# Kernel tuning notes

Measured on AMD Instinct MI355X. Metric: run time of the kernel, lower is better.

## Reference

```python
import jax, jax.numpy as jnp
import numpy as np

N = 100_000   # nodes
D = 128       # in_channels
H = 128       # hidden_channels
O = 128       # out_channels
M = 3_200_000 # adjacency nnz (avg degree 32)
E = 200_000   # query edges
P = 500_000   # common-neighbor pairs (padded, all valid here)
COS_EPS = 1e-8
DEG_EPS = 1e-6


def setup_inputs() -> dict:
    key = jax.random.key(0)
    ks = jax.random.split(key, 12)
    x = jax.random.normal(ks[0], (N, D), jnp.float32)
    adj_row = jnp.sort(jax.random.randint(ks[1], (M,), 0, N, jnp.int32))
    adj_col = jax.random.randint(ks[2], (M,), 0, N, jnp.int32)
    edges = jax.random.randint(ks[3], (2, E), 0, N, jnp.int32)
    cn_edge_idx = jnp.sort(jax.random.randint(ks[4], (P,), 0, E, jnp.int32))
    cn_node = jax.random.randint(ks[5], (P,), 0, N, jnp.int32)
    cn_valid = jnp.ones((P,), jnp.bool_)
    # MLP params (Kaiming-ish scale)
    W1 = jax.random.normal(ks[6], (D, H), jnp.float32) / np.sqrt(D)
    b1 = jnp.zeros((H,), jnp.float32)
    W2 = jax.random.normal(ks[7], (H, H), jnp.float32) / np.sqrt(H)
    b2 = jnp.zeros((H,), jnp.float32)
    W3 = jax.random.normal(ks[8], (H, O), jnp.float32) / np.sqrt(H)
    b3 = jnp.zeros((O,), jnp.float32)
    return dict(x=x, adj_row=adj_row, adj_col=adj_col, edges=edges,
                cn_edge_idx=cn_edge_idx, cn_node=cn_node, cn_valid=cn_valid,
                W1=W1, b1=b1, W2=W2, b2=b2, W3=W3, b3=b3)


def _cosine(a, b):
    # torch.nn.CosineSimilarity: dot / max(||a||*||b||, eps)
    dot = jnp.sum(a * b, axis=-1)
    na = jnp.sqrt(jnp.sum(a * a, axis=-1))
    nb = jnp.sqrt(jnp.sum(b * b, axis=-1))
    return dot / jnp.maximum(na * nb, COS_EPS)


def reference(x, adj_row, adj_col, edges, cn_edge_idx, cn_node, cn_valid,
              W1, b1, W2, b2, W3, b3):
    # degrees = adj.sum(-1) + 1e-6 (binary adjacency values)
    ones = jnp.ones(adj_row.shape[0], x.dtype)
    deg = jax.ops.segment_sum(ones, adj_row, num_segments=N) + DEG_EPS
    # x = x + (adj @ x) / deg[:, None]
    agg = jax.ops.segment_sum(x[adj_col], adj_row, num_segments=N)
    h = x + agg / deg[:, None]
    # MLP (BatchNorms are unused in the original forward; dropout = inference)
    h = jax.nn.relu(h @ W1 + b1)
    h = jax.nn.relu(h @ W2 + b2)
    h = h @ W3 + b3                      # [N, O]
    # gather per common-neighbor pair: u = edges[0][e], v = edges[1][e], c = neighbor
    u = edges[0][cn_edge_idx]
    v = edges[1][cn_edge_idx]
    hu, hv, hc = h[u], h[v], h[cn_node]  # [P, O] each
    w = _cosine(hu, hc) * _cosine(hv, hc)
    w = jnp.where(cn_valid, w, jnp.zeros((), h.dtype))
    # sparse row-sum over neighbors per query edge
    scores = jax.ops.segment_sum(w, cn_edge_idx, num_segments=E)
    return jax.nn.sigmoid(scores)
```

## Files before the change

kernel.cpp:

```cpp
#include <hip/hip_runtime.h>
#include <math.h>

constexpr int N_NODES = 100000;
constexpr int DIM     = 128;
constexpr int M_NNZ   = 3200000;
constexpr int E_EDGES = 200000;
constexpr int P_PAIRS = 500000;
constexpr int W_ELEMS = 3 * DIM * DIM;

typedef _Float16 half8  __attribute__((ext_vector_type(8)));
typedef _Float16 half4t __attribute__((ext_vector_type(4)));
typedef _Float16 half2t __attribute__((ext_vector_type(2)));
typedef float    f32x4  __attribute__((ext_vector_type(4)));
typedef float    f32x2  __attribute__((ext_vector_type(2)));
typedef unsigned int u32x2 __attribute__((ext_vector_type(2)));

#if defined(__has_builtin)
#  if __has_builtin(__builtin_amdgcn_cvt_scalef32_pk8_f16_fp8)
#    define HAVE_PK8 1
#  endif
#endif
#ifndef HAVE_PK8
#  define HAVE_PK8 0
#endif

__device__ inline half8 fp8x8_to_h8(u32x2 d) {
#if HAVE_PK8
    return __builtin_amdgcn_cvt_scalef32_pk8_f16_fp8(d, 1.0f);
#else
    f32x2 p0 = __builtin_amdgcn_cvt_pk_f32_fp8(d[0], false);
    f32x2 p1 = __builtin_amdgcn_cvt_pk_f32_fp8(d[0], true);
    f32x2 p2 = __builtin_amdgcn_cvt_pk_f32_fp8(d[1], false);
    f32x2 p3 = __builtin_amdgcn_cvt_pk_f32_fp8(d[1], true);
    return half8{(_Float16)p0[0], (_Float16)p0[1], (_Float16)p1[0], (_Float16)p1[1],
                 (_Float16)p2[0], (_Float16)p2[1], (_Float16)p3[0], (_Float16)p3[1]};
#endif
}

__device__ inline void stage_weight(const _Float16* __restrict__ src,
                                    _Float16* __restrict__ dst) {
    const int tid = threadIdx.x;
    #pragma unroll
    for (int j = 0; j < 8; ++j) {
        const int gg  = j * 256 + tid;
        const int row = gg >> 4, g = gg & 15;
        *(half8*)(dst + (row << 7) + ((g ^ (row & 15)) << 3)) =
            *(const half8*)(src + gg * 8);
    }
}

__device__ inline half8 ldsw(const _Float16* __restrict__ w,
                             int row, int q, int t, int l16) {
    return *(const half8*)(w + (row << 7) + (((q + 4 * t) ^ l16) << 3));
}

__global__ void prep_kernel(
    const float* __restrict__ W1, const float* __restrict__ W2,
    const float* __restrict__ W3, _Float16* __restrict__ Wt,
    const int* __restrict__ adj_row, int* __restrict__ rs, int* __restrict__ re,
    float* __restrict__ out) {
    const int tid = blockIdx.x * blockDim.x + threadIdx.x;
    if (tid < W_ELEMS) {
        int m = tid >> 14, n = (tid >> 7) & 127, k = tid & 127;
        const float* W = (m == 0) ? W1 : (m == 1) ? W2 : W3;
        Wt[tid] = (_Float16)W[k * DIM + n];
        return;
    }
    if (tid < W_ELEMS + M_NNZ) {
        const int p = tid - W_ELEMS;
        const int v = adj_row[p];
        if (p == 0) {
            rs[v] = 0;
            for (int w = 0; w < v; ++w) { rs[w] = 0; re[w] = 0; }
        } else {
            int pv = adj_row[p - 1];
            if (pv != v) {
                re[pv] = p; rs[v] = p;
                for (int w = pv + 1; w < v; ++w) { rs[w] = p; re[w] = p; }
            }
        }
        if (p == M_NNZ - 1) {
            re[v] = M_NNZ;
            for (int w = v + 1; w < N_NODES; ++w) { rs[w] = M_NNZ; re[w] = M_NNZ; }
        }
        return;
    }
    if (tid < W_ELEMS + M_NNZ + E_EDGES) {
        out[tid - W_ELEMS - M_NNZ] = 0.f;
    }
}

__global__ __launch_bounds__(256) void gemm1_kernel(
    const float* __restrict__ x, const _Float16* __restrict__ Wt,
    _Float16* __restrict__ y, unsigned char* __restrict__ y8) {
    __shared__ __align__(16) _Float16 lw[16384];
    const int lane = threadIdx.x & 63;
    const int wave = threadIdx.x >> 6;
    const int q = lane >> 4, l16 = lane & 15;
    const int rBase = blockIdx.x * 128 + wave * 32;

    const int row0 = rBase + l16, row1 = rBase + 16 + l16;
    const int r0 = min(row0, N_NODES - 1), r1 = min(row1, N_NODES - 1);
    const float* Ap0 = x + (size_t)r0 * DIM + q * 8;
    const float* Ap1 = x + (size_t)r1 * DIM + q * 8;
    half8 a0[4], a1[4];
    #pragma unroll
    for (int t = 0; t < 4; ++t) {
        float4 u0 = *(const float4*)(Ap0 + t * 32);
        float4 u1 = *(const float4*)(Ap0 + t * 32 + 4);
        float4 w0 = *(const float4*)(Ap1 + t * 32);
        float4 w1 = *(const float4*)(Ap1 + t * 32 + 4);
        a0[t] = half8{(_Float16)u0.x, (_Float16)u0.y, (_Float16)u0.z, (_Float16)u0.w,
                      (_Float16)u1.x, (_Float16)u1.y, (_Float16)u1.z, (_Float16)u1.w};
        a1[t] = half8{(_Float16)w0.x, (_Float16)w0.y, (_Float16)w0.z, (_Float16)w0.w,
                      (_Float16)w1.x, (_Float16)w1.y, (_Float16)w1.z, (_Float16)w1.w};
    }
    stage_weight(Wt, lw);
    __syncthreads();

    #pragma unroll
    for (int c = 0; c < 8; ++c) {
        f32x4 acc0 = {0.f, 0.f, 0.f, 0.f}, acc1 = {0.f, 0.f, 0.f, 0.f};
        #pragma unroll
        for (int t = 0; t < 4; ++t) {
            const half8 w = ldsw(lw, c * 16 + l16, q, t, l16);
            acc0 = __builtin_amdgcn_mfma_f32_16x16x32_f16(w, a0[t], acc0, 0, 0, 0);
            acc1 = __builtin_amdgcn_mfma_f32_16x16x32_f16(w, a1[t], acc1, 0, 0, 0);
        }
        const int colBase = c * 16 + q * 4;
        half4t o0 = { (_Float16)acc0[0], (_Float16)acc0[1], (_Float16)acc0[2], (_Float16)acc0[3] };
        half4t o1 = { (_Float16)acc1[0], (_Float16)acc1[1], (_Float16)acc1[2], (_Float16)acc1[3] };
        int p0 = __builtin_amdgcn_cvt_pk_fp8_f32(acc0[0], acc0[1], 0, false);
        p0     = __builtin_amdgcn_cvt_pk_fp8_f32(acc0[2], acc0[3], p0, true);
        int p1 = __builtin_amdgcn_cvt_pk_fp8_f32(acc1[0], acc1[1], 0, false);
        p1     = __builtin_amdgcn_cvt_pk_fp8_f32(acc1[2], acc1[3], p1, true);
        if (row0 < N_NODES) {
            *(half4t*)(y + (size_t)row0 * DIM + colBase) = o0;
            *(int*)(y8 + (size_t)row0 * DIM + colBase) = p0;
        }
        if (row1 < N_NODES) {
            *(half4t*)(y + (size_t)row1 * DIM + colBase) = o1;
            *(int*)(y8 + (size_t)row1 * DIM + colBase) = p1;
        }
    }
}

__global__ __launch_bounds__(256) void agg_kernel(
    const _Float16* __restrict__ y, const unsigned char* __restrict__ y8,
    const int* __restrict__ rs, const int* __restrict__ re,
    const int* __restrict__ adj_col, const float* __restrict__ b1,
    _Float16* __restrict__ h1, int node_base) {
    const int wave = threadIdx.x >> 6, lane = threadIdx.x & 63;
    const int node = node_base + blockIdx.x * 4 + wave;
    const int start = rs[node], cnt = re[node] - start;
    const int g = lane >> 4;
    const int l16 = lane & 15;
    const unsigned b8 = (unsigned)l16 * 8;

    float fa[8];
    half8 a0 = {}, a1 = {}, a2 = {}, a3 = {};
    for (int base = 0; base < cnt; base += 64) {
        const int chunk = min(64, cnt - base);
        const int colreg = adj_col[start + base + min(lane, chunk - 1)];
        int j = 0;
        for (; j + 16 <= chunk; j += 16) {
            int cc[4];
            #pragma unroll
            for (int s = 0; s < 4; ++s) cc[s] = __shfl(colreg, j + 4 * s + g);
            u32x2 dv[4];
            #pragma unroll
            for (int s = 0; s < 4; ++s)
                dv[s] = *(const u32x2*)(y8 + (((unsigned)cc[s] << 7) + b8));
            a0 += fp8x8_to_h8(dv[0]);
            a1 += fp8x8_to_h8(dv[1]);
            a2 += fp8x8_to_h8(dv[2]);
            a3 += fp8x8_to_h8(dv[3]);
        }
        for (; j < chunk; j += 4) {
            const int idx = j + g;
            const int c = __shfl(colreg, min(idx, chunk - 1));
            const u32x2 d = *(const u32x2*)(y8 + (((unsigned)c << 7) + b8));
            const half8 v = fp8x8_to_h8(d);
            if (idx < chunk) a0 += v;
        }
    }
    const half8 hs = (a0 + a1) + (a2 + a3);
    #pragma unroll
    for (int t = 0; t < 8; ++t) fa[t] = (float)hs[t];

    #pragma unroll
    for (int t = 0; t < 8; ++t) {
        float f = fa[t];
        f += __shfl_xor(f, 16);
        f += __shfl_xor(f, 32);
        fa[t] = f;
    }
    if (g == 0) {
        const float inv = 1.f / ((float)cnt + 1e-6f);
        const half8 sf = *(const half8*)(y + (size_t)node * DIM + b8);
        const float4 bb0 = *(const float4*)(b1 + b8);
        const float4 bb1 = *(const float4*)(b1 + b8 + 4);
        half8 o;
        #pragma unroll
        for (int t = 0; t < 8; ++t) {
            const float bb = (t < 4) ? ((const float*)&bb0)[t] : ((const float*)&bb1)[t - 4];
            o[t] = (_Float16)fmaxf((float)sf[t] + fa[t] * inv + bb, 0.f);
        }
        *(half8*)(h1 + (size_t)node * DIM + b8) = o;
    }
}

__global__ __launch_bounds__(256) void mlp23_kernel(
    const _Float16* __restrict__ h1, const _Float16* __restrict__ Wt,
    const float* __restrict__ b2, const float* __restrict__ b3,
    unsigned char* __restrict__ hN8) {
    __shared__ __align__(16) _Float16 lw[16384];
    __shared__ __align__(16) _Float16 tile[4][16][136];
    const int lane = threadIdx.x & 63;
    const int wave = threadIdx.x >> 6;
    const int q = lane >> 4, l16 = lane & 15;
    const int node = blockIdx.x * 64 + wave * 16 + l16;
    const int nl = min(node, N_NODES - 1);

    half8 aF[4];
    #pragma unroll
    for (int t = 0; t < 4; ++t)
        aF[t] = *(const half8*)(h1 + (size_t)nl * DIM + q * 8 + t * 32);

    stage_weight(Wt + 16384, lw);
    __syncthreads();

    half4t o2[8];
    #pragma unroll
    for (int c = 0; c < 8; ++c) {
        f32x4 acc = {0.f, 0.f, 0.f, 0.f};
        #pragma unroll
        for (int t = 0; t < 4; ++t) {
            const half8 w = ldsw(lw, c * 16 + l16, q, t, l16);
            acc = __builtin_amdgcn_mfma_f32_16x16x32_f16(w, aF[t], acc, 0, 0, 0);
        }
        const int colBase = c * 16 + q * 4;
        const float4 bb = *(const float4*)(b2 + colBase);
        o2[c] = half4t{ (_Float16)fmaxf(acc[0] + bb.x, 0.f),
                        (_Float16)fmaxf(acc[1] + bb.y, 0.f),
                        (_Float16)fmaxf(acc[2] + bb.z, 0.f),
                        (_Float16)fmaxf(acc[3] + bb.w, 0.f) };
    }
    __syncthreads();

    stage_weight(Wt + 32768, lw);

    #pragma unroll
    for (int c = 0; c < 8; ++c)
        *(half4t*)(&tile[wave][l16][c * 16 + q * 4]) = o2[c];
    #pragma unroll
    for (int t = 0; t < 4; ++t)
        aF[t] = *(const half8*)(&tile[wave][l16][q * 8 + t * 32]);

    __syncthreads();

    f32x4 vals[8];
    float s = 0.f;
    #pragma unroll
    for (int c = 0; c < 8; ++c) {
        f32x4 acc = {0.f, 0.f, 0.f, 0.f};
        #pragma unroll
        for (int t = 0; t < 4; ++t) {
            const half8 w = ldsw(lw, c * 16 + l16, q, t, l16);
            acc = __builtin_amdgcn_mfma_f32_16x16x32_f16(w, aF[t], acc, 0, 0, 0);
        }
        const int colBase = c * 16 + q * 4;
        const float4 bb = *(const float4*)(b3 + colBase);
        f32x4 v;
        v[0] = acc[0] + bb.x; v[1] = acc[1] + bb.y;
        v[2] = acc[2] + bb.z; v[3] = acc[3] + bb.w;
        s += v[0]*v[0] + v[1]*v[1] + v[2]*v[2] + v[3]*v[3];
        vals[c] = v;
    }
    s += __shfl_xor(s, 16);
    s += __shfl_xor(s, 32);
    const float rn = 1.f / fmaxf(sqrtf(s), 1e-4f);
    if (node < N_NODES) {
        #pragma unroll
        for (int c = 0; c < 8; ++c) {
            const int colBase = c * 16 + q * 4;
            int pk = __builtin_amdgcn_cvt_pk_fp8_f32(vals[c][0] * rn, vals[c][1] * rn, 0, false);
            pk     = __builtin_amdgcn_cvt_pk_fp8_f32(vals[c][2] * rn, vals[c][3] * rn, pk, true);
            *(int*)(hN8 + (((unsigned)node << 7) + colBase)) = pk;
        }
    }
}

__global__ __launch_bounds__(256) void edge_pair_kernel(
    const unsigned char* __restrict__ h8,
    const int* __restrict__ edges, const int* __restrict__ cn_edge,
    const int* __restrict__ cn_node, float* __restrict__ scores) {
    const int lane = threadIdx.x & 63;
    const int wave = threadIdx.x >> 6;
    const int q = lane >> 4, l16 = lane & 15;
    const int pbase = (blockIdx.x * 4 + wave) * 16;
    const int p = pbase + l16;
    const int pc = min(p, P_PAIRS - 1);

    const int e = cn_edge[pc];
    const int c = cn_node[pc];
    const int u = edges[e], v = edges[E_EDGES + e];
    const unsigned off0 = (unsigned)q * 8;

    f32x4 au = {0.f, 0.f, 0.f, 0.f}, av = {0.f, 0.f, 0.f, 0.f};
    #pragma unroll
    for (int t = 0; t < 4; ++t) {
        const unsigned off = off0 + t * 32;
        const half8 hc = fp8x8_to_h8(*(const u32x2*)(h8 + (((unsigned)c << 7) + off)));
        const half8 hu = fp8x8_to_h8(*(const u32x2*)(h8 + (((unsigned)u << 7) + off)));
        const half8 hv = fp8x8_to_h8(*(const u32x2*)(h8 + (((unsigned)v << 7) + off)));
        au = __builtin_amdgcn_mfma_f32_16x16x32_f16(hu, hc, au, 0, 0, 0);
        av = __builtin_amdgcn_mfma_f32_16x16x32_f16(hv, hc, av, 0, 0, 0);
    }
    if ((l16 >> 2) == q && p < P_PAIRS) {
        const int i = l16 & 3;
        atomicAdd(scores + e, au[i] * av[i]);
    }
}

__global__ void sigmoid_kernel(float* __restrict__ out) {
    const int e = blockIdx.x * blockDim.x + threadIdx.x;
    if (e < E_EDGES) out[e] = 1.f / (1.f + expf(-out[e]));
}

extern "C" void kernel_launch(void* const* d_in, const int* in_sizes, int n_in,
                              void* d_out, int out_size, void* d_ws, size_t ws_size,
                              hipStream_t stream) {
    const float* x     = (const float*)d_in[0];
    const int* adj_row = (const int*)d_in[1];
    const int* adj_col = (const int*)d_in[2];
    const int* edges   = (const int*)d_in[3];
    const int* cn_edge = (const int*)d_in[4];
    const int* cn_node = (const int*)d_in[5];
    const float* W1 = (const float*)d_in[7];
    const float* b1 = (const float*)d_in[8];
    const float* W2 = (const float*)d_in[9];
    const float* b2 = (const float*)d_in[10];
    const float* W3 = (const float*)d_in[11];
    const float* b3 = (const float*)d_in[12];
    float* out = (float*)d_out;

    char* base = (char*)d_ws;
    _Float16* y  = (_Float16*)base;
    _Float16* h1 = (_Float16*)(base + 25600000);
    unsigned char* y8 = (unsigned char*)(base + 51200000);
    unsigned char* hN8 = y8;
    _Float16* Wt = (_Float16*)(base + 64000000);
    int* rs = (int*)(base + 64098304);
    int* re = (int*)(base + 64498304);

    const int prep_threads = W_ELEMS + M_NNZ + E_EDGES;
    prep_kernel<<<(prep_threads + 255) / 256, 256, 0, stream>>>(
        W1, W2, W3, Wt, adj_row, rs, re, out);

    gemm1_kernel<<<(N_NODES + 127) / 128, 256, 0, stream>>>(x, Wt, y, y8);
    agg_kernel<<<N_NODES / 16, 256, 0, stream>>>(y, y8, rs, re, adj_col, b1, h1, 0);
    agg_kernel<<<N_NODES / 16, 256, 0, stream>>>(y, y8, rs, re, adj_col, b1, h1, 25000);
    agg_kernel<<<N_NODES / 16, 256, 0, stream>>>(y, y8, rs, re, adj_col, b1, h1, 50000);
    agg_kernel<<<N_NODES / 16, 256, 0, stream>>>(y, y8, rs, re, adj_col, b1, h1, 75000);
    mlp23_kernel<<<(N_NODES + 63) / 64, 256, 0, stream>>>(h1, Wt, b2, b3, hN8);
    edge_pair_kernel<<<(P_PAIRS + 63) / 64, 256, 0, stream>>>(hN8, edges, cn_edge, cn_node, out);
    sigmoid_kernel<<<(E_EDGES + 255) / 256, 256, 0, stream>>>(out);
}
```

Measured before the change: 292.6 us.

## Fuse neighbor aggregation into the MLP kernel via an LDS tile

Merges the four aggregation launches and the layer-2/3 MLP kernel into one. Each wave aggregates 16 nodes one after another and writes the bias-added, ReLU'd rows into a shared-memory tile, which then feeds the MFMA layers directly. This removes the h1 intermediate round trip to global memory and several kernel launches. The cost is that the latency-bound gather now runs inside an LDS-heavy block with serial per-wave node loops, which lowers occupancy for the dominant gather phase. The output buffer is also moved so it no longer aliases y8.

Result: slower. 354.3 us (+21.1%).

```diff
diff --git a/kernel.cpp b/kernel.cpp
--- a/kernel.cpp
+++ b/kernel.cpp
@@ -145,90 +145,84 @@
     }
 }
 
-__global__ __launch_bounds__(256) void agg_kernel(
+__global__ __launch_bounds__(256) void agg_mlp_kernel(
     const _Float16* __restrict__ y, const unsigned char* __restrict__ y8,
     const int* __restrict__ rs, const int* __restrict__ re,
     const int* __restrict__ adj_col, const float* __restrict__ b1,
-    _Float16* __restrict__ h1, int node_base) {
-    const int wave = threadIdx.x >> 6, lane = threadIdx.x & 63;
-    const int node = node_base + blockIdx.x * 4 + wave;
-    const int start = rs[node], cnt = re[node] - start;
-    const int g = lane >> 4;
-    const int l16 = lane & 15;
-    const unsigned b8 = (unsigned)l16 * 8;
-
-    float fa[8];
-    half8 a0 = {}, a1 = {}, a2 = {}, a3 = {};
-    for (int base = 0; base < cnt; base += 64) {
-        const int chunk = min(64, cnt - base);
-        const int colreg = adj_col[start + base + min(lane, chunk - 1)];
-        int j = 0;
-        for (; j + 16 <= chunk; j += 16) {
-            int cc[4];
-            #pragma unroll
-            for (int s = 0; s < 4; ++s) cc[s] = __shfl(colreg, j + 4 * s + g);
-            u32x2 dv[4];
-            #pragma unroll
-            for (int s = 0; s < 4; ++s)
-                dv[s] = *(const u32x2*)(y8 + (((unsigned)cc[s] << 7) + b8));
-            a0 += fp8x8_to_h8(dv[0]);
-            a1 += fp8x8_to_h8(dv[1]);
-            a2 += fp8x8_to_h8(dv[2]);
-            a3 += fp8x8_to_h8(dv[3]);
-        }
-        for (; j < chunk; j += 4) {
-            const int idx = j + g;
-            const int c = __shfl(colreg, min(idx, chunk - 1));
-            const u32x2 d = *(const u32x2*)(y8 + (((unsigned)c << 7) + b8));
-            const half8 v = fp8x8_to_h8(d);
-            if (idx < chunk) a0 += v;
-        }
-    }
-    const half8 hs = (a0 + a1) + (a2 + a3);
-    #pragma unroll
-    for (int t = 0; t < 8; ++t) fa[t] = (float)hs[t];
-
-    #pragma unroll
-    for (int t = 0; t < 8; ++t) {
-        float f = fa[t];
-        f += __shfl_xor(f, 16);
-        f += __shfl_xor(f, 32);
-        fa[t] = f;
-    }
-    if (g == 0) {
-        const float inv = 1.f / ((float)cnt + 1e-6f);
-        const half8 sf = *(const half8*)(y + (size_t)node * DIM + b8);
-        const float4 bb0 = *(const float4*)(b1 + b8);
-        const float4 bb1 = *(const float4*)(b1 + b8 + 4);
-        half8 o;
-        #pragma unroll
-        for (int t = 0; t < 8; ++t) {
-            const float bb = (t < 4) ? ((const float*)&bb0)[t] : ((const float*)&bb1)[t - 4];
-            o[t] = (_Float16)fmaxf((float)sf[t] + fa[t] * inv + bb, 0.f);
-        }
-        *(half8*)(h1 + (size_t)node * DIM + b8) = o;
-    }
-}
-
-__global__ __launch_bounds__(256) void mlp23_kernel(
-    const _Float16* __restrict__ h1, const _Float16* __restrict__ Wt,
-    const float* __restrict__ b2, const float* __restrict__ b3,
-    unsigned char* __restrict__ hN8) {
+    const _Float16* __restrict__ Wt, const float* __restrict__ b2,
+    const float* __restrict__ b3, unsigned char* __restrict__ hN8) {
     __shared__ __align__(16) _Float16 lw[16384];
     __shared__ __align__(16) _Float16 tile[4][16][136];
     const int lane = threadIdx.x & 63;
     const int wave = threadIdx.x >> 6;
     const int q = lane >> 4, l16 = lane & 15;
-    const int node = blockIdx.x * 64 + wave * 16 + l16;
-    const int nl = min(node, N_NODES - 1);
+    const int g = q;
+    const unsigned b8 = (unsigned)l16 * 8;
+    const int rBase = blockIdx.x * 64 + wave * 16;
+
+    stage_weight(Wt + 16384, lw);
+
+    const float4 bb0 = *(const float4*)(b1 + b8);
+    const float4 bb1 = *(const float4*)(b1 + b8 + 4);
+    for (int n = 0; n < 16; ++n) {
+        const int node = min(rBase + n, N_NODES - 1);
+        const int start = rs[node], cnt = re[node] - start;
+
+        half8 a0 = {}, a1 = {}, a2 = {}, a3 = {};
+        for (int base = 0; base < cnt; base += 64) {
+            const int chunk = min(64, cnt - base);
+            const int colreg = adj_col[start + base + min(lane, chunk - 1)];
+            int j = 0;
+            for (; j + 16 <= chunk; j += 16) {
+                int cc[4];
+                #pragma unroll
+                for (int s = 0; s < 4; ++s) cc[s] = __shfl(colreg, j + 4 * s + g);
+                u32x2 dv[4];
+                #pragma unroll
+                for (int s = 0; s < 4; ++s)
+                    dv[s] = *(const u32x2*)(y8 + (((unsigned)cc[s] << 7) + b8));
+                a0 += fp8x8_to_h8(dv[0]);
+                a1 += fp8x8_to_h8(dv[1]);
+                a2 += fp8x8_to_h8(dv[2]);
+                a3 += fp8x8_to_h8(dv[3]);
+            }
+            for (; j < chunk; j += 4) {
+                const int idx = j + g;
+                const int c = __shfl(colreg, min(idx, chunk - 1));
+                const u32x2 d = *(const u32x2*)(y8 + (((unsigned)c << 7) + b8));
+                const half8 v = fp8x8_to_h8(d);
+                if (idx < chunk) a0 += v;
+            }
+        }
+        const half8 hs = (a0 + a1) + (a2 + a3);
+        float fa[8];
+        #pragma unroll
+        for (int t = 0; t < 8; ++t) fa[t] = (float)hs[t];
+        #pragma unroll
+        for (int t = 0; t < 8; ++t) {
+            float f = fa[t];
+            f += __shfl_xor(f, 16);
+            f += __shfl_xor(f, 32);
+            fa[t] = f;
+        }
+        if (g == 0) {
+            const float inv = 1.f / ((float)cnt + 1e-6f);
+            const half8 sf = *(const half8*)(y + (size_t)node * DIM + b8);
+            half8 o;
+            #pragma unroll
+            for (int t = 0; t < 8; ++t) {
+                const float bb = (t < 4) ? ((const float*)&bb0)[t] : ((const float*)&bb1)[t - 4];
+                o[t] = (_Float16)fmaxf((float)sf[t] + fa[t] * inv + bb, 0.f);
+            }
+            *(half8*)(&tile[wave][n][l16 * 8]) = o;
+        }
+    }
+    __syncthreads();
 
     half8 aF[4];
     #pragma unroll
     for (int t = 0; t < 4; ++t)
-        aF[t] = *(const half8*)(h1 + (size_t)nl * DIM + q * 8 + t * 32);
-
-    stage_weight(Wt + 16384, lw);
-    __syncthreads();
+        aF[t] = *(const half8*)(&tile[wave][l16][q * 8 + t * 32]);
 
     half4t o2[8];
     #pragma unroll
@@ -280,13 +274,14 @@
     s += __shfl_xor(s, 16);
     s += __shfl_xor(s, 32);
     const float rn = 1.f / fmaxf(sqrtf(s), 1e-4f);
-    if (node < N_NODES) {
+    const int nodeOut = rBase + l16;
+    if (nodeOut < N_NODES) {
         #pragma unroll
         for (int c = 0; c < 8; ++c) {
             const int colBase = c * 16 + q * 4;
             int pk = __builtin_amdgcn_cvt_pk_fp8_f32(vals[c][0] * rn, vals[c][1] * rn, 0, false);
             pk     = __builtin_amdgcn_cvt_pk_fp8_f32(vals[c][2] * rn, vals[c][3] * rn, pk, true);
-            *(int*)(hN8 + (((unsigned)node << 7) + colBase)) = pk;
+            *(int*)(hN8 + (((unsigned)nodeOut << 7) + colBase)) = pk;
         }
     }
 }
@@ -347,9 +342,8 @@
 
     char* base = (char*)d_ws;
     _Float16* y  = (_Float16*)base;
-    _Float16* h1 = (_Float16*)(base + 25600000);
+    unsigned char* hN8 = (unsigned char*)(base + 25600000);
     unsigned char* y8 = (unsigned char*)(base + 51200000);
-    unsigned char* hN8 = y8;
     _Float16* Wt = (_Float16*)(base + 64000000);
     int* rs = (int*)(base + 64098304);
     int* re = (int*)(base + 64498304);
@@ -359,11 +353,8 @@
         W1, W2, W3, Wt, adj_row, rs, re, out);
 
     gemm1_kernel<<<(N_NODES + 127) / 128, 256, 0, stream>>>(x, Wt, y, y8);
-    agg_kernel<<<N_NODES / 16, 256, 0, stream>>>(y, y8, rs, re, adj_col, b1, h1, 0);
-    agg_kernel<<<N_NODES / 16, 256, 0, stream>>>(y, y8, rs, re, adj_col, b1, h1, 25000);
-    agg_kernel<<<N_NODES / 16, 256, 0, stream>>>(y, y8, rs, re, adj_col, b1, h1, 50000);
-    agg_kernel<<<N_NODES / 16, 256, 0, stream>>>(y, y8, rs, re, adj_col, b1, h1, 75000);
-    mlp23_kernel<<<(N_NODES + 63) / 64, 256, 0, stream>>>(h1, Wt, b2, b3, hN8);
+    agg_mlp_kernel<<<(N_NODES + 63) / 64, 256, 0, stream>>>(
+        y, y8, rs, re, adj_col, b1, Wt, b2, b3, hN8);
     edge_pair_kernel<<<(P_PAIRS + 63) / 64, 256, 0, stream>>>(hN8, edges, cn_edge, cn_node, out);
     sigmoid_kernel<<<(E_EDGES + 255) / 256, 256, 0, stream>>>(out);
 }
```
